# Performance work log

Hardware: AMD Instinct MI355X
Metric: run time of the kernel (lower is better)

The kernel has to match this reference:

```python
import jax, jax.numpy as jnp
import numpy as np

N = 100000
E = 1600000
IN_C, HID_C, OUT_C = 64, 128, 64


def sage_conv(x, edge_index, W_l, b_l, W_r):
    # PyG SAGEConv (mean aggr): out = lin_l(mean_{j in N(i)} x_j) + lin_r(x_i)
    src, dst = edge_index[0], edge_index[1]
    n = x.shape[0]
    msg = x[src]                                        # [E, C] gather
    agg = jax.ops.segment_sum(msg, dst, num_segments=n) # [N, C] scatter-add
    deg = jax.ops.segment_sum(jnp.ones((msg.shape[0],), x.dtype), dst, num_segments=n)
    agg = agg / jnp.maximum(deg, 1.0)[:, None]          # mean, deg-0 safe
    return agg @ W_l.T + b_l + x @ W_r.T


def setup_inputs() -> dict:
    key = jax.random.key(0)
    ks = jax.random.split(key, 8)
    x = jax.random.normal(ks[0], (N, IN_C), dtype=jnp.float32)
    edge_index = jax.random.randint(ks[1], (2, E), 0, N)
    s1 = 1.0 / np.sqrt(IN_C)
    s2 = 1.0 / np.sqrt(HID_C)
    W1_l = jax.random.uniform(ks[2], (HID_C, IN_C), jnp.float32, -s1, s1)
    W1_r = jax.random.uniform(ks[3], (HID_C, IN_C), jnp.float32, -s1, s1)
    b1 = jax.random.uniform(ks[4], (HID_C,), jnp.float32, -s1, s1)
    W2_l = jax.random.uniform(ks[5], (OUT_C, HID_C), jnp.float32, -s2, s2)
    W2_r = jax.random.uniform(ks[6], (OUT_C, HID_C), jnp.float32, -s2, s2)
    b2 = jax.random.uniform(ks[7], (OUT_C,), jnp.float32, -s2, s2)
    return {"x": x, "edge_index": edge_index, "W1_l": W1_l, "W1_r": W1_r,
            "b1": b1, "W2_l": W2_l, "W2_r": W2_r, "b2": b2}


def reference(x, edge_index, W1_l, W1_r, b1, W2_l, W2_r, b2):
    h = sage_conv(x, edge_index, W1_l, b1, W1_r)
    h = jax.nn.relu(h)
    h = sage_conv(h, edge_index, W2_l, b2, W2_r)
    return jax.nn.sigmoid(h)
```

## Files before the change

kernel.cpp:

```cpp
#include <hip/hip_runtime.h>
#include <math.h>

#define IN_C 64
#define HID_C 128
#define OUT_C 64
#define NBK 256
#define BD 64
#define GS 16

typedef __attribute__((ext_vector_type(8))) short bf16x8;
typedef __attribute__((ext_vector_type(4))) float f32x4;

__device__ __forceinline__ unsigned short f2bf(float f) {
  unsigned u = __float_as_uint(f);
  u = (u + 0x7FFFu + ((u >> 16) & 1u)) >> 16;
  return (unsigned short)u;
}
__device__ __forceinline__ float bf2f(unsigned v) {
  return __uint_as_float(v << 16);
}
__device__ __forceinline__ unsigned pack2(float a, float b) {
  return (unsigned)f2bf(a) | ((unsigned)f2bf(b) << 16);
}

__global__ __launch_bounds__(256) void k_xcast(const float4* __restrict__ x4,
                                               uint2* __restrict__ xh2,
                                               int Mreal, int Mtot) {
  for (int i = blockIdx.x * 256 + threadIdx.x; i < Mtot; i += gridDim.x * 256) {
    uint2 p = {0u, 0u};
    if (i < Mreal) {
      float4 v = x4[i];
      p.x = pack2(v.x, v.y);
      p.y = pack2(v.z, v.w);
    }
    xh2[i] = p;
  }
}

__global__ __launch_bounds__(256) void k_bhistL(const int* __restrict__ dst,
                                                int* __restrict__ bh, int E) {
  __shared__ int h[NBK];
  int t = threadIdx.x;
  h[t] = 0;
  __syncthreads();
  for (int e = blockIdx.x * 256 + t; e < E; e += gridDim.x * 256)
    atomicAdd(&h[dst[e] >> 9], 1);
  __syncthreads();
  if (h[t]) atomicAdd(&bh[t * GS], h[t]);
}

__global__ __launch_bounds__(256) void k_bscan(const int* __restrict__ bh,
                                               int* __restrict__ bstart,
                                               int* __restrict__ rstart,
                                               int* __restrict__ gcur) {
  __shared__ int s1[NBK], s2[NBK];
  int t = threadIdx.x;
  int cnt = bh[t * GS];
  int region = 16 * min(cnt, (cnt >> 4) + 512);
  int creg = cnt + 4096;
  s1[t] = region; s2[t] = creg;
  __syncthreads();
  for (int off = 1; off < NBK; off <<= 1) {
    int a1 = (t >= off) ? s1[t - off] : 0;
    int a2 = (t >= off) ? s2[t - off] : 0;
    __syncthreads();
    s1[t] += a1; s2[t] += a2;
    __syncthreads();
  }
  int ex1 = s1[t] - region;
  int ex2 = s2[t] - creg;
  bstart[t] = ex1; gcur[t * GS] = ex1; rstart[t] = ex2;
}

__global__ __launch_bounds__(256) void k_msplit(const int* __restrict__ src,
                                                const int* __restrict__ dst,
                                                int* __restrict__ gcur,
                                                int* __restrict__ ebuf, int E) {
  __shared__ int bcnt[NBK], bhead[NBK];
  __shared__ int bins[BD][NBK];
  int t = threadIdx.x;
  bcnt[t] = 0; bhead[t] = 0;
  int per = (E + gridDim.x - 1) / gridDim.x;
  int e0 = blockIdx.x * per, e1 = min(E, e0 + per);
  int e = e0 + t;
  int pb[4], pv[4]; int pc = 0;
  __syncthreads();
  for (;;) {
    while (pc < 4 && e < e1) {
      int d = dst[e], s = src[e];
      pb[pc] = d >> 9; pv[pc] = (s << 9) | (d & 511);
      pc++; e += 256;
    }
    for (int q = pc - 1; q >= 0; --q) {
      int pos = atomicAdd(&bcnt[pb[q]], 1);
      if (pos < BD) {
        bins[(bhead[pb[q]] + pos) & (BD - 1)][pb[q]] = pv[q];
        pc--;
        if (q != pc) { pb[q] = pb[pc]; pv[q] = pv[pc]; }
      }
    }
    int pending = __syncthreads_count(pc > 0 || e < e1);
    int cntv = min(bcnt[t], BD);
    int head = bhead[t];
    while (cntv >= 16) {
      int base = atomicAdd(&gcur[t * GS], 16);
      int4 o[4];
#pragma unroll
      for (int k = 0; k < 16; ++k)
        ((int*)o)[k] = bins[(head + k) & (BD - 1)][t];
      int4* g = (int4*)(ebuf + base);
      g[0] = o[0]; g[1] = o[1]; g[2] = o[2]; g[3] = o[3];
      head = (head + 16) & (BD - 1);
      cntv -= 16;
    }
    bhead[t] = head;
    bcnt[t] = cntv;
    __syncthreads();
    if (!pending) break;
  }
  int cntv = bcnt[t];
  if (cntv > 0) {
    int head = bhead[t];
    int base = atomicAdd(&gcur[t * GS], 16);
#pragma unroll
    for (int k = 0; k < 16; ++k)
      ebuf[base + k] = (k < cntv) ? bins[(head + k) & (BD - 1)][t] : -1;
  }
}

__global__ __launch_bounds__(512) void k_localcsr(const int* __restrict__ ebuf,
                                                  const int* __restrict__ bstart,
                                                  const int* __restrict__ gcur,
                                                  const int* __restrict__ rstart,
                                                  int* __restrict__ csr,
                                                  int* __restrict__ row_start,
                                                  int* __restrict__ rend,
                                                  float* __restrict__ invd, int N) {
  __shared__ int lcnt[512], loff[512], lcur[512];
  int t = threadIdx.x, b = blockIdx.x;
  int start = bstart[b], endp = gcur[b * GS], rs = rstart[b];
  lcnt[t] = 0;
  __syncthreads();
  for (int i = start + t; i < endp; i += 512) {
    int pe = ebuf[i];
    if (pe != -1) atomicAdd(&lcnt[pe & 511], 1);
  }
  __syncthreads();
  int v = lcnt[t];
  int pvn = (v + 7) & ~7;
  loff[t] = pvn;
  __syncthreads();
  for (int off = 1; off < 512; off <<= 1) {
    int a = (t >= off) ? loff[t - off] : 0;
    __syncthreads();
    loff[t] += a;
    __syncthreads();
  }
  int ex = loff[t] - pvn;
  lcur[t] = ex;
  int node = (b << 9) + t;
  if (node < N) {
    row_start[node] = rs + ex;
    rend[node] = rs + ex + pvn;
    invd[node] = 1.0f / fmaxf((float)v, 1.0f);
  }
  __syncthreads();
  for (int i = start + t; i < endp; i += 512) {
    int pe = ebuf[i];
    if (pe != -1) {
      int pos = atomicAdd(&lcur[pe & 511], 1);
      csr[rs + pos] = pe >> 9;
    }
  }
  for (int k = ex + v; k < ex + pvn; ++k) csr[rs + k] = N;
}

__global__ __launch_bounds__(256) void k_gather1(const uint4* __restrict__ xh4,
                                                 const int* __restrict__ csr,
                                                 const int* __restrict__ row_start,
                                                 const int* __restrict__ rend,
                                                 const float* __restrict__ invd,
                                                 uint4* __restrict__ aggh4, int N) {
  int wid = (blockIdx.x * blockDim.x + threadIdx.x) >> 6;
  int lane = threadIdx.x & 63;
  if (wid >= N) return;
  int rq = lane >> 3, cq = lane & 7;
  int j = row_start[wid], end = rend[wid];
  float a0 = 0, a1 = 0, a2 = 0, a3 = 0, a4 = 0, a5 = 0, a6 = 0, a7 = 0;
#pragma unroll 2
  for (; j < end; j += 8) {
    int s = csr[j + rq];
    uint4 v = xh4[s * 8 + cq];
    a0 += bf2f(v.x & 0xffffu); a1 += bf2f(v.x >> 16);
    a2 += bf2f(v.y & 0xffffu); a3 += bf2f(v.y >> 16);
    a4 += bf2f(v.z & 0xffffu); a5 += bf2f(v.z >> 16);
    a6 += bf2f(v.w & 0xffffu); a7 += bf2f(v.w >> 16);
  }
#define RED8(d)                                               \
  a0 += __shfl_xor(a0, d); a1 += __shfl_xor(a1, d);           \
  a2 += __shfl_xor(a2, d); a3 += __shfl_xor(a3, d);           \
  a4 += __shfl_xor(a4, d); a5 += __shfl_xor(a5, d);           \
  a6 += __shfl_xor(a6, d); a7 += __shfl_xor(a7, d);
  RED8(8) RED8(16) RED8(32)
  if (rq == 0) {
    float inv = invd[wid];
    uint4 p;
    p.x = pack2(a0 * inv, a1 * inv);
    p.y = pack2(a2 * inv, a3 * inv);
    p.z = pack2(a4 * inv, a5 * inv);
    p.w = pack2(a6 * inv, a7 * inv);
    aggh4[wid * 8 + cq] = p;
  }
}

__global__ __launch_bounds__(256, 3) void k_lin1(
    const unsigned short* __restrict__ aggh, const unsigned short* __restrict__ xh,
    const float* __restrict__ W1l, const float* __restrict__ W1r,
    const float* __restrict__ b1, unsigned short* __restrict__ h, int N) {
  __shared__ __align__(16) unsigned short sW[128 * 136];
  __shared__ __align__(16) unsigned short sA[64 * 136];
  __shared__ float sb[128];
  int t = threadIdx.x;
  for (int i = t; i < 128 * 128; i += 256) {
    int o = i >> 7, k = i & 127;
    float w = (k < 64) ? W1l[o * 64 + k] : W1r[o * 64 + (k - 64)];
    sW[o * 136 + k] = f2bf(w);
  }
  if (t < 128) sb[t] = b1[t];
  int lane = t & 63, qm = lane >> 4, ln = lane & 15;
  int m0 = (t >> 6) * 16;
  __syncthreads();

  int ntiles = (N + 63) >> 6;
  for (int tile = blockIdx.x; tile < ntiles; tile += gridDim.x) {
    int base = tile << 6;
    for (int u = t; u < 64 * 64; u += 256) {
      int n = u >> 6, uu = u & 63;
      int node = base + n;
      unsigned v = 0;
      if (node < N) v = (uu < 32) ? ((const unsigned*)aggh)[node * 32 + uu]
                                  : ((const unsigned*)xh)[node * 32 + (uu - 32)];
      ((unsigned*)(sA + n * 136))[uu] = v;
    }
    __syncthreads();
    bf16x8 af[4];
#pragma unroll
    for (int kc = 0; kc < 4; ++kc)
      af[kc] = *(const bf16x8*)(sA + (m0 + ln) * 136 + kc * 32 + qm * 8);
#pragma unroll
    for (int ot = 0; ot < 8; ++ot) {
      int o0 = ot * 16;
      f32x4 acc = {0.f, 0.f, 0.f, 0.f};
#pragma unroll
      for (int kc = 0; kc < 4; ++kc) {
        bf16x8 bfr = *(const bf16x8*)(sW + (o0 + ln) * 136 + kc * 32 + qm * 8);
        acc = __builtin_amdgcn_mfma_f32_16x16x32_bf16(af[kc], bfr, acc, 0, 0, 0);
      }
      int col = o0 + ln;
      float bias = sb[col];
#pragma unroll
      for (int i = 0; i < 4; ++i) {
        int node = base + m0 + qm * 4 + i;
        if (node < N) h[node * 128 + col] = f2bf(fmaxf(acc[i] + bias, 0.f));
      }
    }
    __syncthreads();
  }
}

__global__ __launch_bounds__(256, 3) void k_lin2(
    const unsigned short* __restrict__ h, const float* __restrict__ W2l,
    const float* __restrict__ W2r, const float* __restrict__ b2,
    unsigned short* __restrict__ zh, float* __restrict__ r, int N) {
  __shared__ __align__(16) unsigned short sW[128 * 136];
  __shared__ __align__(16) unsigned short sA[64 * 136];
  __shared__ float sb2[64];
  int t = threadIdx.x;
  if (blockIdx.x == 0 && t < 32) ((unsigned*)zh)[N * 32 + t] = 0;
  for (int i = t; i < 128 * 128; i += 256) {
    int u = i >> 7, k = i & 127;
    float w = (u < 64) ? W2l[u * 128 + k] : W2r[(u - 64) * 128 + k];
    sW[u * 136 + k] = f2bf(w);
  }
  if (t < 64) sb2[t] = b2[t];
  int lane = t & 63, qm = lane >> 4, ln = lane & 15;
  int m0 = (t >> 6) * 16;
  __syncthreads();

  int ntiles = (N + 63) >> 6;
  for (int tile = blockIdx.x; tile < ntiles; tile += gridDim.x) {
    int base = tile << 6;
    for (int u = t; u < 64 * 64; u += 256) {
      int n = u >> 6, uu = u & 63;
      int node = base + n;
      unsigned v = 0;
      if (node < N) v = ((const unsigned*)h)[node * 64 + uu];
      ((unsigned*)(sA + n * 136))[uu] = v;
    }
    __syncthreads();
    bf16x8 af[4];
#pragma unroll
    for (int kc = 0; kc < 4; ++kc)
      af[kc] = *(const bf16x8*)(sA + (m0 + ln) * 136 + kc * 32 + qm * 8);
#pragma unroll
    for (int ot = 0; ot < 8; ++ot) {
      int o0 = ot * 16;
      f32x4 acc = {0.f, 0.f, 0.f, 0.f};
#pragma unroll
      for (int kc = 0; kc < 4; ++kc) {
        bf16x8 bfr = *(const bf16x8*)(sW + (o0 + ln) * 136 + kc * 32 + qm * 8);
        acc = __builtin_amdgcn_mfma_f32_16x16x32_bf16(af[kc], bfr, acc, 0, 0, 0);
      }
      int u = o0 + ln;
#pragma unroll
      for (int i = 0; i < 4; ++i) {
        int node = base + m0 + qm * 4 + i;
        if (node < N) {
          if (u < 64) zh[node * 64 + u] = f2bf(acc[i]);
          else        r[node * 64 + (u - 64)] = acc[i] + sb2[u - 64];
        }
      }
    }
    __syncthreads();
  }
}

__global__ __launch_bounds__(256) void k_gather2b(const uint4* __restrict__ zh4,
                                                  const float* __restrict__ r,
                                                  const int* __restrict__ csr,
                                                  const int* __restrict__ row_start,
                                                  const int* __restrict__ rend,
                                                  const float* __restrict__ invd,
                                                  float* __restrict__ out, int N) {
  int wid = (blockIdx.x * blockDim.x + threadIdx.x) >> 6;
  int lane = threadIdx.x & 63;
  if (wid >= N) return;
  int rq = lane >> 3, cq = lane & 7;
  int j = row_start[wid], end = rend[wid];
  float a0 = 0, a1 = 0, a2 = 0, a3 = 0, a4 = 0, a5 = 0, a6 = 0, a7 = 0;
#pragma unroll 2
  for (; j < end; j += 8) {
    int s = csr[j + rq];
    uint4 v = zh4[s * 8 + cq];
    a0 += bf2f(v.x & 0xffffu); a1 += bf2f(v.x >> 16);
    a2 += bf2f(v.y & 0xffffu); a3 += bf2f(v.y >> 16);
    a4 += bf2f(v.z & 0xffffu); a5 += bf2f(v.z >> 16);
    a6 += bf2f(v.w & 0xffffu); a7 += bf2f(v.w >> 16);
  }
  RED8(8) RED8(16) RED8(32)
  if (rq == 0) {
    float inv = invd[wid];
    const float4* r4 = (const float4*)r;
    float4 rv0 = r4[wid * 16 + cq * 2];
    float4 rv1 = r4[wid * 16 + cq * 2 + 1];
    float4 o0, o1;
    o0.x = 1.0f / (1.0f + __expf(-(a0 * inv + rv0.x)));
    o0.y = 1.0f / (1.0f + __expf(-(a1 * inv + rv0.y)));
    o0.z = 1.0f / (1.0f + __expf(-(a2 * inv + rv0.z)));
    o0.w = 1.0f / (1.0f + __expf(-(a3 * inv + rv0.w)));
    o1.x = 1.0f / (1.0f + __expf(-(a4 * inv + rv1.x)));
    o1.y = 1.0f / (1.0f + __expf(-(a5 * inv + rv1.y)));
    o1.z = 1.0f / (1.0f + __expf(-(a6 * inv + rv1.z)));
    o1.w = 1.0f / (1.0f + __expf(-(a7 * inv + rv1.w)));
    float4* out4 = (float4*)out;
    out4[wid * 16 + cq * 2] = o0;
    out4[wid * 16 + cq * 2 + 1] = o1;
  }
}

extern "C" void kernel_launch(void* const* d_in, const int* in_sizes, int n_in,
                              void* d_out, int out_size, void* d_ws, size_t ws_size,
                              hipStream_t stream) {
  const float* x   = (const float*)d_in[0];
  const int*   ei  = (const int*)d_in[1];
  const float* W1l = (const float*)d_in[2];
  const float* W1r = (const float*)d_in[3];
  const float* b1  = (const float*)d_in[4];
  const float* W2l = (const float*)d_in[5];
  const float* W2r = (const float*)d_in[6];
  const float* b2  = (const float*)d_in[7];
  float* out = (float*)d_out;

  int N = in_sizes[0] / IN_C;
  int E = in_sizes[1] / 2;
  const int* src = ei;
  const int* dst = ei + E;

  char* ws = (char*)d_ws;
  size_t off = 0;
  auto alignup = [](size_t v) { return (v + 511) & ~(size_t)511; };
  int* bh = (int*)(ws + off);         off = alignup(off + NBK * GS * 4);
  int* gcur = (int*)(ws + off);       off = alignup(off + NBK * GS * 4);
  int* bstart = (int*)(ws + off);     off = alignup(off + NBK * 4);
  int* rstart = (int*)(ws + off);     off = alignup(off + NBK * 4);
  int* csr = (int*)(ws + off);        off = alignup(off + ((size_t)E + NBK * 4096) * 4);
  int* row_start = (int*)(ws + off);  off = alignup(off + (size_t)N * 4);
  int* rend = (int*)(ws + off);       off = alignup(off + (size_t)N * 4);
  float* invd = (float*)(ws + off);   off = alignup(off + (size_t)N * 4);
  unsigned short* xh = (unsigned short*)(ws + off);   off = alignup(off + (size_t)(N + 1) * 64 * 2);
  unsigned short* aggh = (unsigned short*)(ws + off); off = alignup(off + (size_t)N * 64 * 2);
  unsigned short* zh = (unsigned short*)(ws + off);   off = alignup(off + (size_t)(N + 1) * 64 * 2);
  float* rbuf = (float*)(ws + off);   off = alignup(off + (size_t)N * 64 * 4);
  unsigned short* hbuf = (unsigned short*)(ws + off);
  int* ebuf = (int*)aggh;

  hipMemsetAsync(bh, 0, NBK * GS * 4, stream);
  k_xcast<<<2048, 256, 0, stream>>>((const float4*)x, (uint2*)xh, N * 16, (N + 1) * 16);
  k_bhistL<<<1024, 256, 0, stream>>>(dst, bh, E);
  k_bscan<<<1, NBK, 0, stream>>>(bh, bstart, rstart, gcur);
  k_msplit<<<512, 256, 0, stream>>>(src, dst, gcur, ebuf, E);
  k_localcsr<<<NBK, 512, 0, stream>>>(ebuf, bstart, gcur, rstart, csr,
                                      row_start, rend, invd, N);

  k_gather1<<<(N + 3) / 4, 256, 0, stream>>>((const uint4*)xh, csr, row_start,
                                             rend, invd, (uint4*)aggh, N);
  k_lin1<<<768, 256, 0, stream>>>(aggh, xh, W1l, W1r, b1, hbuf, N);
  k_lin2<<<768, 256, 0, stream>>>(hbuf, W2l, W2r, b2, zh, rbuf, N);
  k_gather2b<<<(N + 3) / 4, 256, 0, stream>>>((const uint4*)zh, rbuf, csr,
                                              row_start, rend, invd, out, N);
}
```

Baseline: 307.9 us.

## Fuse layer-1 gather into linear kernel, merge cast with histogram, widen msplit buffer

Merges the x-to-bf16 cast and the destination histogram into one launch, with block ranges split between the two tasks. Folds the layer-1 neighbour gather into the MFMA linear kernel: each wave aggregates its 16 rows into shared memory and reads the self features straight from global, which removes the aggh round trip and one launch. Also raises the per-thread pending-edge buffer in msplit from 4 to 8, and makes the final gather epilogue write all 64 lanes with coalesced scalar stores instead of 8 lanes storing float4. The fused kernel runs only 768 persistent blocks for a latency-bound gather, which may expose less memory parallelism than the old one-wave-per-node launch.

New measurement: 353.5 us. 14.8% more time.

```diff
diff --git a/kernel.cpp b/kernel.cpp
--- a/kernel.cpp
+++ b/kernel.cpp
@@ -23,30 +23,38 @@
   return (unsigned)f2bf(a) | ((unsigned)f2bf(b) << 16);
 }
 
-__global__ __launch_bounds__(256) void k_xcast(const float4* __restrict__ x4,
-                                               uint2* __restrict__ xh2,
-                                               int Mreal, int Mtot) {
-  for (int i = blockIdx.x * 256 + threadIdx.x; i < Mtot; i += gridDim.x * 256) {
-    uint2 p = {0u, 0u};
-    if (i < Mreal) {
-      float4 v = x4[i];
-      p.x = pack2(v.x, v.y);
-      p.y = pack2(v.z, v.w);
-    }
-    xh2[i] = p;
-  }
-}
-
-__global__ __launch_bounds__(256) void k_bhistL(const int* __restrict__ dst,
-                                                int* __restrict__ bh, int E) {
-  __shared__ int h[NBK];
+#define RED8(d)                                               \
+  a0 += __shfl_xor(a0, d); a1 += __shfl_xor(a1, d);           \
+  a2 += __shfl_xor(a2, d); a3 += __shfl_xor(a3, d);           \
+  a4 += __shfl_xor(a4, d); a5 += __shfl_xor(a5, d);           \
+  a6 += __shfl_xor(a6, d); a7 += __shfl_xor(a7, d);
+
+__global__ __launch_bounds__(256) void k_xb(const int* __restrict__ dst,
+                                            int* __restrict__ bh,
+                                            const float4* __restrict__ x4,
+                                            uint2* __restrict__ xh2,
+                                            int E, int Mreal, int Mtot) {
+  __shared__ int hh[NBK];
   int t = threadIdx.x;
-  h[t] = 0;
-  __syncthreads();
-  for (int e = blockIdx.x * 256 + t; e < E; e += gridDim.x * 256)
-    atomicAdd(&h[dst[e] >> 9], 1);
-  __syncthreads();
-  if (h[t]) atomicAdd(&bh[t * GS], h[t]);
+  if (blockIdx.x < 1024) {
+    hh[t] = 0;
+    __syncthreads();
+    for (int e = blockIdx.x * 256 + t; e < E; e += 1024 * 256)
+      atomicAdd(&hh[dst[e] >> 9], 1);
+    __syncthreads();
+    if (hh[t]) atomicAdd(&bh[t * GS], hh[t]);
+  } else {
+    int b = blockIdx.x - 1024;
+    for (int i = b * 256 + t; i < Mtot; i += 2048 * 256) {
+      uint2 p = {0u, 0u};
+      if (i < Mreal) {
+        float4 v = x4[i];
+        p.x = pack2(v.x, v.y);
+        p.y = pack2(v.z, v.w);
+      }
+      xh2[i] = p;
+    }
+  }
 }
 
 __global__ __launch_bounds__(256) void k_bscan(const int* __restrict__ bh,
@@ -83,10 +91,10 @@
   int per = (E + gridDim.x - 1) / gridDim.x;
   int e0 = blockIdx.x * per, e1 = min(E, e0 + per);
   int e = e0 + t;
-  int pb[4], pv[4]; int pc = 0;
+  int pb[8], pv[8]; int pc = 0;
   __syncthreads();
   for (;;) {
-    while (pc < 4 && e < e1) {
+    while (pc < 8 && e < e1) {
       int d = dst[e], s = src[e];
       pb[pc] = d >> 9; pv[pc] = (s << 9) | (d & 511);
       pc++; e += 256;
@@ -175,50 +183,14 @@
   for (int k = ex + v; k < ex + pvn; ++k) csr[rs + k] = N;
 }
 
-__global__ __launch_bounds__(256) void k_gather1(const uint4* __restrict__ xh4,
-                                                 const int* __restrict__ csr,
-                                                 const int* __restrict__ row_start,
-                                                 const int* __restrict__ rend,
-                                                 const float* __restrict__ invd,
-                                                 uint4* __restrict__ aggh4, int N) {
-  int wid = (blockIdx.x * blockDim.x + threadIdx.x) >> 6;
-  int lane = threadIdx.x & 63;
-  if (wid >= N) return;
-  int rq = lane >> 3, cq = lane & 7;
-  int j = row_start[wid], end = rend[wid];
-  float a0 = 0, a1 = 0, a2 = 0, a3 = 0, a4 = 0, a5 = 0, a6 = 0, a7 = 0;
-#pragma unroll 2
-  for (; j < end; j += 8) {
-    int s = csr[j + rq];
-    uint4 v = xh4[s * 8 + cq];
-    a0 += bf2f(v.x & 0xffffu); a1 += bf2f(v.x >> 16);
-    a2 += bf2f(v.y & 0xffffu); a3 += bf2f(v.y >> 16);
-    a4 += bf2f(v.z & 0xffffu); a5 += bf2f(v.z >> 16);
-    a6 += bf2f(v.w & 0xffffu); a7 += bf2f(v.w >> 16);
-  }
-#define RED8(d)                                               \
-  a0 += __shfl_xor(a0, d); a1 += __shfl_xor(a1, d);           \
-  a2 += __shfl_xor(a2, d); a3 += __shfl_xor(a3, d);           \
-  a4 += __shfl_xor(a4, d); a5 += __shfl_xor(a5, d);           \
-  a6 += __shfl_xor(a6, d); a7 += __shfl_xor(a7, d);
-  RED8(8) RED8(16) RED8(32)
-  if (rq == 0) {
-    float inv = invd[wid];
-    uint4 p;
-    p.x = pack2(a0 * inv, a1 * inv);
-    p.y = pack2(a2 * inv, a3 * inv);
-    p.z = pack2(a4 * inv, a5 * inv);
-    p.w = pack2(a6 * inv, a7 * inv);
-    aggh4[wid * 8 + cq] = p;
-  }
-}
-
-__global__ __launch_bounds__(256, 3) void k_lin1(
-    const unsigned short* __restrict__ aggh, const unsigned short* __restrict__ xh,
+__global__ __launch_bounds__(256, 3) void k_gl1(
+    const unsigned short* __restrict__ xh, const int* __restrict__ csr,
+    const int* __restrict__ row_start, const int* __restrict__ rend,
+    const float* __restrict__ invd,
     const float* __restrict__ W1l, const float* __restrict__ W1r,
     const float* __restrict__ b1, unsigned short* __restrict__ h, int N) {
   __shared__ __align__(16) unsigned short sW[128 * 136];
-  __shared__ __align__(16) unsigned short sA[64 * 136];
+  __shared__ __align__(16) unsigned short sA[64 * 72];
   __shared__ float sb[128];
   int t = threadIdx.x;
   for (int i = t; i < 128 * 128; i += 256) {
@@ -228,25 +200,47 @@
   }
   if (t < 128) sb[t] = b1[t];
   int lane = t & 63, qm = lane >> 4, ln = lane & 15;
+  int rq = lane >> 3, cq = lane & 7;
   int m0 = (t >> 6) * 16;
+  const uint4* xh4 = (const uint4*)xh;
   __syncthreads();
 
   int ntiles = (N + 63) >> 6;
   for (int tile = blockIdx.x; tile < ntiles; tile += gridDim.x) {
     int base = tile << 6;
-    for (int u = t; u < 64 * 64; u += 256) {
-      int n = u >> 6, uu = u & 63;
-      int node = base + n;
-      unsigned v = 0;
-      if (node < N) v = (uu < 32) ? ((const unsigned*)aggh)[node * 32 + uu]
-                                  : ((const unsigned*)xh)[node * 32 + (uu - 32)];
-      ((unsigned*)(sA + n * 136))[uu] = v;
-    }
-    __syncthreads();
+    for (int n = 0; n < 16; ++n) {
+      int node = base + m0 + n;
+      if (node >= N) break;
+      int j = row_start[node], end = rend[node];
+      float a0 = 0, a1 = 0, a2 = 0, a3 = 0, a4 = 0, a5 = 0, a6 = 0, a7 = 0;
+#pragma unroll 2
+      for (; j < end; j += 8) {
+        int s = csr[j + rq];
+        uint4 v = xh4[s * 8 + cq];
+        a0 += bf2f(v.x & 0xffffu); a1 += bf2f(v.x >> 16);
+        a2 += bf2f(v.y & 0xffffu); a3 += bf2f(v.y >> 16);
+        a4 += bf2f(v.z & 0xffffu); a5 += bf2f(v.z >> 16);
+        a6 += bf2f(v.w & 0xffffu); a7 += bf2f(v.w >> 16);
+      }
+      RED8(8) RED8(16) RED8(32)
+      if (rq == 0) {
+        float inv = invd[node];
+        uint4 p;
+        p.x = pack2(a0 * inv, a1 * inv);
+        p.y = pack2(a2 * inv, a3 * inv);
+        p.z = pack2(a4 * inv, a5 * inv);
+        p.w = pack2(a6 * inv, a7 * inv);
+        *(uint4*)(sA + (m0 + n) * 72 + cq * 8) = p;
+      }
+    }
+    int arow = m0 + ln;
+    int anode = base + arow;
+    int axnode = min(anode, N);
     bf16x8 af[4];
-#pragma unroll
-    for (int kc = 0; kc < 4; ++kc)
-      af[kc] = *(const bf16x8*)(sA + (m0 + ln) * 136 + kc * 32 + qm * 8);
+    af[0] = *(const bf16x8*)(sA + arow * 72 + qm * 8);
+    af[1] = *(const bf16x8*)(sA + arow * 72 + 32 + qm * 8);
+    af[2] = *(const bf16x8*)(xh + axnode * 64 + qm * 8);
+    af[3] = *(const bf16x8*)(xh + axnode * 64 + 32 + qm * 8);
 #pragma unroll
     for (int ot = 0; ot < 8; ++ot) {
       int o0 = ot * 16;
@@ -264,7 +258,6 @@
         if (node < N) h[node * 128 + col] = f2bf(fmaxf(acc[i] + bias, 0.f));
       }
     }
-    __syncthreads();
   }
 }
 
@@ -348,24 +341,14 @@
     a6 += bf2f(v.w & 0xffffu); a7 += bf2f(v.w >> 16);
   }
   RED8(8) RED8(16) RED8(32)
-  if (rq == 0) {
-    float inv = invd[wid];
-    const float4* r4 = (const float4*)r;
-    float4 rv0 = r4[wid * 16 + cq * 2];
-    float4 rv1 = r4[wid * 16 + cq * 2 + 1];
-    float4 o0, o1;
-    o0.x = 1.0f / (1.0f + __expf(-(a0 * inv + rv0.x)));
-    o0.y = 1.0f / (1.0f + __expf(-(a1 * inv + rv0.y)));
-    o0.z = 1.0f / (1.0f + __expf(-(a2 * inv + rv0.z)));
-    o0.w = 1.0f / (1.0f + __expf(-(a3 * inv + rv0.w)));
-    o1.x = 1.0f / (1.0f + __expf(-(a4 * inv + rv1.x)));
-    o1.y = 1.0f / (1.0f + __expf(-(a5 * inv + rv1.y)));
-    o1.z = 1.0f / (1.0f + __expf(-(a6 * inv + rv1.z)));
-    o1.w = 1.0f / (1.0f + __expf(-(a7 * inv + rv1.w)));
-    float4* out4 = (float4*)out;
-    out4[wid * 16 + cq * 2] = o0;
-    out4[wid * 16 + cq * 2 + 1] = o1;
-  }
+  bool s0 = (rq & 1) != 0, s1 = (rq & 2) != 0, s2 = (rq & 4) != 0;
+  float t0 = s0 ? a1 : a0, t1 = s0 ? a3 : a2;
+  float t2 = s0 ? a5 : a4, t3 = s0 ? a7 : a6;
+  float u0 = s1 ? t1 : t0, u1 = s1 ? t3 : t2;
+  float vsum = s2 ? u1 : u0;
+  int c = cq * 8 + rq;
+  float pre = vsum * invd[wid] + r[wid * 64 + c];
+  out[wid * 64 + c] = 1.0f / (1.0f + __expf(-pre));
 }
 
 extern "C" void kernel_launch(void* const* d_in, const int* in_sizes, int n_in,
@@ -397,24 +380,22 @@
   int* row_start = (int*)(ws + off);  off = alignup(off + (size_t)N * 4);
   int* rend = (int*)(ws + off);       off = alignup(off + (size_t)N * 4);
   float* invd = (float*)(ws + off);   off = alignup(off + (size_t)N * 4);
-  unsigned short* xh = (unsigned short*)(ws + off);   off = alignup(off + (size_t)(N + 1) * 64 * 2);
-  unsigned short* aggh = (unsigned short*)(ws + off); off = alignup(off + (size_t)N * 64 * 2);
-  unsigned short* zh = (unsigned short*)(ws + off);   off = alignup(off + (size_t)(N + 1) * 64 * 2);
+  unsigned short* xh = (unsigned short*)(ws + off); off = alignup(off + (size_t)(N + 1) * 64 * 2);
+  unsigned short* zh = (unsigned short*)(ws + off); off = alignup(off + (size_t)(N + 1) * 64 * 2);
   float* rbuf = (float*)(ws + off);   off = alignup(off + (size_t)N * 64 * 4);
   unsigned short* hbuf = (unsigned short*)(ws + off);
-  int* ebuf = (int*)aggh;
+  int* ebuf = (int*)zh;
 
   hipMemsetAsync(bh, 0, NBK * GS * 4, stream);
-  k_xcast<<<2048, 256, 0, stream>>>((const float4*)x, (uint2*)xh, N * 16, (N + 1) * 16);
-  k_bhistL<<<1024, 256, 0, stream>>>(dst, bh, E);
+  k_xb<<<3072, 256, 0, stream>>>(dst, bh, (const float4*)x, (uint2*)xh,
+                                 E, N * 16, (N + 1) * 16);
   k_bscan<<<1, NBK, 0, stream>>>(bh, bstart, rstart, gcur);
   k_msplit<<<512, 256, 0, stream>>>(src, dst, gcur, ebuf, E);
   k_localcsr<<<NBK, 512, 0, stream>>>(ebuf, bstart, gcur, rstart, csr,
                                       row_start, rend, invd, N);
 
-  k_gather1<<<(N + 3) / 4, 256, 0, stream>>>((const uint4*)xh, csr, row_start,
-                                             rend, invd, (uint4*)aggh, N);
-  k_lin1<<<768, 256, 0, stream>>>(aggh, xh, W1l, W1r, b1, hbuf, N);
+  k_gl1<<<768, 256, 0, stream>>>(xh, csr, row_start, rend, invd,
+                                 W1l, W1r, b1, hbuf, N);
   k_lin2<<<768, 256, 0, stream>>>(hbuf, W2l, W2r, b2, zh, rbuf, N);
   k_gather2b<<<(N + 3) / 4, 256, 0, stream>>>((const uint4*)zh, rbuf, csr,
                                               row_start, rend, invd, out, N);
```
